# Kernel optimization log

Measured on AMD Instinct MI355X. Metric: run time of the kernel, lower is better.

Reference implementation:

```python
import jax, jax.numpy as jnp
import numpy as np

B, L, K = 4096, 4096, 10


def _sparsemax(z):
    # z: [..., n]; Martins & Astudillo sparsemax along last dim
    n = z.shape[-1]
    zs = -jnp.sort(-z, axis=-1)                      # descending
    cum = jnp.cumsum(zs, axis=-1)
    r = jnp.arange(1, n + 1, dtype=z.dtype)
    support = (1.0 + r * zs) > cum                   # [..., n]
    ksel = jnp.sum(support, axis=-1, keepdims=True)  # support size
    tau = (jnp.take_along_axis(cum, ksel - 1, axis=-1) - 1.0) / ksel.astype(z.dtype)
    return jnp.maximum(z - tau, 0.0)


def _topk_bitvectors(logits, k):
    # k highest-scoring binary vectors z in {0,1}^L under <z, logits>
    # (faithful to the CPU batched_topk: detached logits)
    lg = jax.lax.stop_gradient(logits)
    b, latent = lg.shape
    base = (lg > 0).astype(lg.dtype)                 # argmax config [B, L]
    costs = jnp.abs(lg)                              # flip costs
    neg_small, pos = jax.lax.top_k(-costs, k)        # k smallest costs + positions
    c_small = -neg_small                             # [B, k]
    m = 1 << k                                       # 2^k candidate flip subsets
    bits = ((jnp.arange(m)[:, None] >> jnp.arange(k)[None, :]) & 1).astype(lg.dtype)  # [2^k, k]
    sums = jnp.einsum('mk,bk->bm', bits, c_small)    # total flip cost per subset
    _, best = jax.lax.top_k(-sums, k)                # k cheapest subsets [B, k]
    flips = bits[best]                               # [B, k, k] which small-cost bits to flip
    base_at = jnp.take_along_axis(base, pos, axis=1) # base bit value at flip positions [B, k]
    delta = flips * (1.0 - 2.0 * base_at[:, None, :])  # +1 or -1 where flipped
    bv = jnp.broadcast_to(base[:, None, :], (b, k, latent))
    bidx = jnp.arange(b)[:, None, None]
    cidx = jnp.arange(k)[None, :, None]
    jpos = pos[:, None, :]                           # [B, 1, k]
    bv = bv.at[bidx, cidx, jpos].add(delta)          # scatter flips -> [B, k, L]
    return bv


def reference(logits, k):
    bv = _topk_bitvectors(logits, k)                         # [B, k, L]
    scores = jnp.einsum('bkj,bj->bk', bv, logits)            # [B, k]
    distr = _sparsemax(scores)                               # [B, k]
    p = distr.reshape(-1)
    safe_p = jnp.where(p > 0, p, 1.0)
    entropy = -jnp.sum(jnp.where(p > 0, p * jnp.log(safe_p), 0.0))
    batch_size = logits.shape[0]
    return bv, distr, entropy / batch_size


def setup_inputs() -> dict:
    key = jax.random.key(0)
    logits = jax.random.normal(key, (B, L), dtype=jnp.float32)
    return {"logits": logits, "k": K}
```

## Files before the change

kernel.cpp:

```cpp
#include <hip/hip_runtime.h>
#include <stdint.h>

#define NB   4096
#define LDIM 4096
#define KK   10
#define TPB  256
#define CAP  1024

typedef float fx4 __attribute__((ext_vector_type(4)));

__device__ __forceinline__ unsigned long long wave_min_u64(unsigned long long v) {
#pragma unroll
    for (int off = 1; off < 64; off <<= 1) {
        const unsigned long long o = __shfl_xor(v, off, 64);
        if (o < v) v = o;
    }
    return v;
}

__global__ __launch_bounds__(TPB) void select_rows(
    const float* __restrict__ logits,
    float* __restrict__ distr,
    float* __restrict__ entp,
    unsigned* __restrict__ meta)
{
    __shared__ float s_wsum[4];
    __shared__ int   s_pos[KK];
    __shared__ int   s_sign[KK];
    __shared__ int   s_bestm[KK];
    __shared__ int   s_cnt;
    __shared__ unsigned long long s_cand[CAP];

    const int b    = blockIdx.x;
    const int t    = threadIdx.x;
    const int lane = t & 63;
    const int wv   = t >> 6;
    const float* __restrict__ row = logits + (size_t)b * LDIM;

    float vals[16];
#pragma unroll
    for (int q = 0; q < 4; q++) {
        const float4 f = *(const float4*)(row + (q << 10) + (t << 2));
        vals[q*4+0] = f.x; vals[q*4+1] = f.y; vals[q*4+2] = f.z; vals[q*4+3] = f.w;
    }

    float s0 = 0.f;
#pragma unroll
    for (int i = 0; i < 16; i++) s0 += vals[i] > 0.f ? vals[i] : 0.f;
#pragma unroll
    for (int off = 1; off < 64; off <<= 1) s0 += __shfl_xor(s0, off, 64);
    if (lane == 0) s_wsum[wv] = s0;

    float T = 0.02f;
    int cnt = 0;
    for (int attempt = 0; attempt < 15; attempt++) {
        if (t == 0) s_cnt = 0;
        __syncthreads();
#pragma unroll
        for (int i = 0; i < 16; i++) {
            const float v    = vals[i];
            const float cost = fabsf(v);
            if (cost < T) {
                const int idx = ((i >> 2) << 10) + (t << 2) + (i & 3);
                const unsigned long long pk =
                    ((unsigned long long)__float_as_uint(cost) << 32)
                    | (unsigned)((idx << 1) | (v > 0.f ? 1 : 0));
                const int p = atomicAdd(&s_cnt, 1);
                if (p < CAP) s_cand[p] = pk;
            }
        }
        __syncthreads();
        cnt = s_cnt;
        if (cnt >= KK && cnt <= CAP) break;
        T = (cnt < KK) ? T * 4.0f : T * 0.25f;
        __syncthreads();
    }

    if (wv != 0) return;

    const float S0 = (s_wsum[0] + s_wsum[1]) + (s_wsum[2] + s_wsum[3]);
    float csm[KK];
    unsigned long long prev = 0ull;

    if (cnt >= KK && cnt <= CAP) {
        const int nc = cnt;
#pragma unroll
        for (int c = 0; c < KK; c++) {
            unsigned long long best = ~0ull;
            for (int p = lane; p < nc; p += 64) {
                const unsigned long long pk = s_cand[p];
                if ((c == 0 || pk > prev) && pk < best) best = pk;
            }
            best = wave_min_u64(best);
            prev = best;
            csm[c] = __uint_as_float((unsigned)(best >> 32));
            if (lane == 0) {
                const unsigned lo = (unsigned)best;
                s_pos[c]  = (int)(lo >> 1);
                s_sign[c] = (int)(lo & 1u);
            }
        }
    } else {
#pragma unroll
        for (int c = 0; c < KK; c++) {
            unsigned long long best = ~0ull;
            for (int p = lane; p < LDIM; p += 64) {
                const float v    = row[p];
                const float cost = fabsf(v);
                const unsigned long long pk =
                    ((unsigned long long)__float_as_uint(cost) << 32)
                    | (unsigned)((p << 1) | (v > 0.f ? 1 : 0));
                if ((c == 0 || pk > prev) && pk < best) best = pk;
            }
            best = wave_min_u64(best);
            prev = best;
            csm[c] = __uint_as_float((unsigned)(best >> 32));
            if (lane == 0) {
                const unsigned lo = (unsigned)best;
                s_pos[c]  = (int)(lo >> 1);
                s_sign[c] = (int)(lo & 1u);
            }
        }
    }

    float sums[16];
#pragma unroll
    for (int i = 0; i < 16; i++) {
        const int m = (lane << 4) | i;
        float acc = 0.f;
#pragma unroll
        for (int j = 0; j < KK; j++) acc += (m & (1 << j)) ? csm[j] : 0.f;
        sums[i] = acc;
    }

    float zc[KK];
    unsigned long long prev2 = 0ull;
#pragma unroll
    for (int c = 0; c < KK; c++) {
        unsigned long long best = ~0ull;
#pragma unroll
        for (int i = 0; i < 16; i++) {
            const unsigned long long pk =
                ((unsigned long long)__float_as_uint(sums[i]) << 32)
                | (unsigned)((lane << 4) | i);
            if ((c == 0 || pk > prev2) && pk < best) best = pk;
        }
        best = wave_min_u64(best);
        prev2 = best;
        zc[c] = S0 - __uint_as_float((unsigned)(best >> 32));
        if (lane == 0) s_bestm[c] = (int)((unsigned)best & 1023u);
    }

    if (lane == 0) {
        float acc = 0.f; int ks = 0;
#pragma unroll
        for (int r = 1; r <= KK; r++) {
            acc += zc[r-1];
            if (1.f + (float)r * zc[r-1] > acc) ks++;
        }
        float acc2 = 0.f;
#pragma unroll
        for (int r = 0; r < KK; r++) if (r < ks) acc2 += zc[r];
        const float tau = (acc2 - 1.f) / (float)ks;
        float entl = 0.f;
        float* drow = distr + b * KK;
#pragma unroll
        for (int c = 0; c < KK; c++) {
            float p = zc[c] - tau;
            p = p > 0.f ? p : 0.f;
            drow[c] = p;
            if (p > 0.f) entl -= p * logf(p);
        }
        entp[b] = entl;

        unsigned* mrow = meta + b * KK;
#pragma unroll
        for (int s = 0; s < KK; s++) {
            unsigned fm = 0u;
#pragma unroll
            for (int c = 0; c < KK; c++)
                fm |= (((unsigned)s_bestm[c] >> s) & 1u) << c;
            mrow[s] = (unsigned)s_pos[s] | (fm << 12) | ((unsigned)s_sign[s] << 22);
        }
    }
}

__global__ __launch_bounds__(TPB) void bv_writer(
    const float* __restrict__ logits,
    const unsigned* __restrict__ meta,
    float* __restrict__ bv)
{
    __shared__ unsigned s_m[KK];
    const int bid = blockIdx.x;
    const int b   = bid >> 2;
    const int seg = bid & 3;
    const int t   = threadIdx.x;
    if (t < KK) s_m[t] = meta[b * KK + t];
    __syncthreads();

    const int j0 = (seg << 10) + (t << 2);
    const float4 f = *(const float4*)(logits + (size_t)b * LDIM + j0);
    float basef[4];
    basef[0] = f.x > 0.f ? 1.f : 0.f;
    basef[1] = f.y > 0.f ? 1.f : 0.f;
    basef[2] = f.z > 0.f ? 1.f : 0.f;
    basef[3] = f.w > 0.f ? 1.f : 0.f;

    unsigned rf[4] = {0u, 0u, 0u, 0u};
    float    fv[4] = {0.f, 0.f, 0.f, 0.f};
#pragma unroll
    for (int s = 0; s < KK; s++) {
        const unsigned m   = s_m[s];
        const int      pos = (int)(m & 0xFFFu);
        const unsigned msk = (m >> 12) & 0x3FFu;
        const float    val = ((m >> 22) & 1u) ? 0.f : 1.f;
#pragma unroll
        for (int e = 0; e < 4; e++)
            if (pos == j0 + e) { rf[e] = msk; fv[e] = val; }
    }

    float* out0 = bv + (size_t)b * (KK * LDIM) + j0;
#pragma unroll
    for (int c = 0; c < KK; c++) {
        fx4 v;
        v.x = ((rf[0] >> c) & 1u) ? fv[0] : basef[0];
        v.y = ((rf[1] >> c) & 1u) ? fv[1] : basef[1];
        v.z = ((rf[2] >> c) & 1u) ? fv[2] : basef[2];
        v.w = ((rf[3] >> c) & 1u) ? fv[3] : basef[3];
        __builtin_nontemporal_store(v, (fx4*)(out0 + c * LDIM));
    }
}

__global__ __launch_bounds__(256) void ent_reduce(
    const float* __restrict__ ws, float* __restrict__ ent)
{
    __shared__ float sw[4];
    const int t = threadIdx.x, lane = t & 63, wv = t >> 6;
    float s = 0.f;
    for (int i = t; i < NB; i += 256) s += ws[i];
#pragma unroll
    for (int off = 1; off < 64; off <<= 1) s += __shfl_xor(s, off, 64);
    if (lane == 0) sw[wv] = s;
    __syncthreads();
    if (t == 0) *ent = (sw[0] + sw[1] + sw[2] + sw[3]) * (1.0f / (float)NB);
}

__global__ __launch_bounds__(TPB) void topk_sparsemax_fused(
    const float* __restrict__ logits,
    float* __restrict__ bv,
    float* __restrict__ distr,
    float* __restrict__ ent)
{
    __shared__ float s_wsum[4];
    __shared__ int   s_pos[KK];
    __shared__ int   s_sign[KK];
    __shared__ int   s_bestm[KK];
    __shared__ int   s_cnt;
    __shared__ unsigned long long s_cand[CAP];

    const int b    = blockIdx.x;
    const int t    = threadIdx.x;
    const int lane = t & 63;
    const int wv   = t >> 6;
    const float* __restrict__ row = logits + (size_t)b * LDIM;

    float vals[16];
#pragma unroll
    for (int q = 0; q < 4; q++) {
        const float4 f = *(const float4*)(row + (q << 10) + (t << 2));
        vals[q*4+0] = f.x; vals[q*4+1] = f.y; vals[q*4+2] = f.z; vals[q*4+3] = f.w;
    }

    float s0 = 0.f;
#pragma unroll
    for (int i = 0; i < 16; i++) s0 += vals[i] > 0.f ? vals[i] : 0.f;
#pragma unroll
    for (int off = 1; off < 64; off <<= 1) s0 += __shfl_xor(s0, off, 64);
    if (lane == 0) s_wsum[wv] = s0;

    float T = 0.02f;
    int cnt = 0;
    for (int attempt = 0; attempt < 15; attempt++) {
        if (t == 0) s_cnt = 0;
        __syncthreads();
#pragma unroll
        for (int i = 0; i < 16; i++) {
            const float v    = vals[i];
            const float cost = fabsf(v);
            if (cost < T) {
                const int idx = ((i >> 2) << 10) + (t << 2) + (i & 3);
                const unsigned long long pk =
                    ((unsigned long long)__float_as_uint(cost) << 32)
                    | (unsigned)((idx << 1) | (v > 0.f ? 1 : 0));
                const int p = atomicAdd(&s_cnt, 1);
                if (p < CAP) s_cand[p] = pk;
            }
        }
        __syncthreads();
        cnt = s_cnt;
        if (cnt >= KK && cnt <= CAP) break;
        T = (cnt < KK) ? T * 4.0f : T * 0.25f;
        __syncthreads();
    }

    if (wv == 0) {
        const float S0 = (s_wsum[0] + s_wsum[1]) + (s_wsum[2] + s_wsum[3]);
        float csm[KK];
        unsigned long long prev = 0ull;
        if (cnt >= KK && cnt <= CAP) {
            const int nc = cnt;
#pragma unroll
            for (int c = 0; c < KK; c++) {
                unsigned long long best = ~0ull;
                for (int p = lane; p < nc; p += 64) {
                    const unsigned long long pk = s_cand[p];
                    if ((c == 0 || pk > prev) && pk < best) best = pk;
                }
                best = wave_min_u64(best);
                prev = best;
                csm[c] = __uint_as_float((unsigned)(best >> 32));
                if (lane == 0) {
                    const unsigned lo = (unsigned)best;
                    s_pos[c]  = (int)(lo >> 1);
                    s_sign[c] = (int)(lo & 1u);
                }
            }
        } else {
#pragma unroll
            for (int c = 0; c < KK; c++) {
                unsigned long long best = ~0ull;
                for (int p = lane; p < LDIM; p += 64) {
                    const float v    = row[p];
                    const float cost = fabsf(v);
                    const unsigned long long pk =
                        ((unsigned long long)__float_as_uint(cost) << 32)
                        | (unsigned)((p << 1) | (v > 0.f ? 1 : 0));
                    if ((c == 0 || pk > prev) && pk < best) best = pk;
                }
                best = wave_min_u64(best);
                prev = best;
                csm[c] = __uint_as_float((unsigned)(best >> 32));
                if (lane == 0) {
                    const unsigned lo = (unsigned)best;
                    s_pos[c]  = (int)(lo >> 1);
                    s_sign[c] = (int)(lo & 1u);
                }
            }
        }
        float sums[16];
#pragma unroll
        for (int i = 0; i < 16; i++) {
            const int m = (lane << 4) | i;
            float acc = 0.f;
#pragma unroll
            for (int j = 0; j < KK; j++) acc += (m & (1 << j)) ? csm[j] : 0.f;
            sums[i] = acc;
        }
        float zc[KK];
        unsigned long long prev2 = 0ull;
#pragma unroll
        for (int c = 0; c < KK; c++) {
            unsigned long long best = ~0ull;
#pragma unroll
            for (int i = 0; i < 16; i++) {
                const unsigned long long pk =
                    ((unsigned long long)__float_as_uint(sums[i]) << 32)
                    | (unsigned)((lane << 4) | i);
                if ((c == 0 || pk > prev2) && pk < best) best = pk;
            }
            best = wave_min_u64(best);
            prev2 = best;
            zc[c] = S0 - __uint_as_float((unsigned)(best >> 32));
            if (lane == 0) s_bestm[c] = (int)((unsigned)best & 1023u);
        }
        if (lane == 0) {
            float acc = 0.f; int ks = 0;
#pragma unroll
            for (int r = 1; r <= KK; r++) {
                acc += zc[r-1];
                if (1.f + (float)r * zc[r-1] > acc) ks++;
            }
            float acc2 = 0.f;
#pragma unroll
            for (int r = 0; r < KK; r++) if (r < ks) acc2 += zc[r];
            const float tau = (acc2 - 1.f) / (float)ks;
            float entl = 0.f;
            float* drow = distr + b * KK;
#pragma unroll
            for (int c = 0; c < KK; c++) {
                float p = zc[c] - tau;
                p = p > 0.f ? p : 0.f;
                drow[c] = p;
                if (p > 0.f) entl -= p * logf(p);
            }
            atomicAdd(ent, entl * (1.0f / (float)NB));
        }
    }

    __syncthreads();

    unsigned fm[KK];
#pragma unroll
    for (int j = 0; j < KK; j++) {
        unsigned m = 0u;
#pragma unroll
        for (int c = 0; c < KK; c++)
            m |= (((unsigned)s_bestm[c] >> j) & 1u) << c;
        fm[j] = m;
    }
    int posr[KK], sgnr[KK];
#pragma unroll
    for (int j = 0; j < KK; j++) { posr[j] = s_pos[j]; sgnr[j] = s_sign[j]; }

    unsigned rowflip[16]; float flipval[16]; float basef[16];
#pragma unroll
    for (int i = 0; i < 16; i++) {
        const int col = ((i >> 2) << 10) + (t << 2) + (i & 3);
        unsigned rfm = 0u; float fvv = 0.f;
#pragma unroll
        for (int j = 0; j < KK; j++) {
            if (posr[j] == col) { rfm = fm[j]; fvv = sgnr[j] ? 0.f : 1.f; }
        }
        rowflip[i] = rfm; flipval[i] = fvv;
        basef[i]   = vals[i] > 0.f ? 1.f : 0.f;
    }

    float* out0 = bv + (size_t)b * (KK * LDIM);
#pragma unroll
    for (int c = 0; c < KK; c++) {
        float* orow = out0 + c * LDIM + (t << 2);
#pragma unroll
        for (int q = 0; q < 4; q++) {
            fx4 v;
            v.x = ((rowflip[q*4+0] >> c) & 1u) ? flipval[q*4+0] : basef[q*4+0];
            v.y = ((rowflip[q*4+1] >> c) & 1u) ? flipval[q*4+1] : basef[q*4+1];
            v.z = ((rowflip[q*4+2] >> c) & 1u) ? flipval[q*4+2] : basef[q*4+2];
            v.w = ((rowflip[q*4+3] >> c) & 1u) ? flipval[q*4+3] : basef[q*4+3];
            __builtin_nontemporal_store(v, (fx4*)(orow + (q << 10)));
        }
    }
}

extern "C" void kernel_launch(void* const* d_in, const int* in_sizes, int n_in,
                              void* d_out, int out_size, void* d_ws, size_t ws_size,
                              hipStream_t stream)
{
    const float* logits = (const float*)d_in[0];
    float* out   = (float*)d_out;
    float* bv    = out;
    float* distr = out + (size_t)NB * KK * LDIM;
    float* ent   = distr + (size_t)NB * KK;

    const size_t need = (size_t)NB * sizeof(float)
                      + (size_t)NB * KK * sizeof(unsigned);
    if (ws_size >= need) {
        float*    entp = (float*)d_ws;
        unsigned* meta = (unsigned*)((float*)d_ws + NB);
        select_rows<<<dim3(NB), dim3(TPB), 0, stream>>>(logits, distr, entp, meta);
        bv_writer <<<dim3(NB * 4), dim3(TPB), 0, stream>>>(logits, meta, bv);
        ent_reduce<<<dim3(1), dim3(256), 0, stream>>>(entp, ent);
    } else {
        (void)hipMemsetAsync(ent, 0, sizeof(float), stream);
        topk_sparsemax_fused<<<dim3(NB), dim3(TPB), 0, stream>>>(logits, bv, distr, ent);
    }
}
```

Measured before the change: 701.1 us.

## Pack base sign bits in select pass; bv writer reads bitmask instead of logits

```diff
diff --git a/kernel.cpp b/kernel.cpp
--- a/kernel.cpp
+++ b/kernel.cpp
@@ -22,13 +22,15 @@
     const float* __restrict__ logits,
     float* __restrict__ distr,
     float* __restrict__ entp,
-    unsigned* __restrict__ meta)
+    unsigned* __restrict__ meta,
+    unsigned* __restrict__ basebits)
 {
     __shared__ float s_wsum[4];
     __shared__ int   s_pos[KK];
     __shared__ int   s_sign[KK];
     __shared__ int   s_bestm[KK];
     __shared__ int   s_cnt;
+    __shared__ unsigned s_base[128];
     __shared__ unsigned long long s_cand[CAP];
 
     const int b    = blockIdx.x;
@@ -50,6 +52,17 @@
 #pragma unroll
     for (int off = 1; off < 64; off <<= 1) s0 += __shfl_xor(s0, off, 64);
     if (lane == 0) s_wsum[wv] = s0;
+
+    if (t < 128) s_base[t] = 0u;
+    __syncthreads();
+#pragma unroll
+    for (int q = 0; q < 4; q++) {
+        unsigned nib = 0u;
+#pragma unroll
+        for (int e = 0; e < 4; e++)
+            nib |= (vals[q*4+e] > 0.f ? 1u : 0u) << e;
+        atomicOr(&s_base[(q << 5) + (t >> 3)], nib << (4 * (t & 7)));
+    }
 
     float T = 0.02f;
     int cnt = 0;
@@ -76,6 +89,8 @@
         __syncthreads();
     }
 
+    if (t < 128) basebits[b * 128 + t] = s_base[t];
+
     if (wv != 0) return;
 
     const float S0 = (s_wsum[0] + s_wsum[1]) + (s_wsum[2] + s_wsum[3]);
@@ -186,48 +201,43 @@
 }
 
 __global__ __launch_bounds__(TPB) void bv_writer(
-    const float* __restrict__ logits,
+    const unsigned* __restrict__ basebits,
     const unsigned* __restrict__ meta,
     float* __restrict__ bv)
 {
+    __shared__ unsigned s_base[128];
     __shared__ unsigned s_m[KK];
-    const int bid = blockIdx.x;
-    const int b   = bid >> 2;
-    const int seg = bid & 3;
-    const int t   = threadIdx.x;
-    if (t < KK) s_m[t] = meta[b * KK + t];
+    const int c = blockIdx.x;
+    const int b = blockIdx.y;
+    const int t = threadIdx.x;
+
+    if (t < 128) s_base[t] = basebits[b * 128 + t];
+    else if (t < 128 + KK) s_m[t - 128] = meta[b * KK + (t - 128)];
     __syncthreads();
 
-    const int j0 = (seg << 10) + (t << 2);
-    const float4 f = *(const float4*)(logits + (size_t)b * LDIM + j0);
-    float basef[4];
-    basef[0] = f.x > 0.f ? 1.f : 0.f;
-    basef[1] = f.y > 0.f ? 1.f : 0.f;
-    basef[2] = f.z > 0.f ? 1.f : 0.f;
-    basef[3] = f.w > 0.f ? 1.f : 0.f;
-
-    unsigned rf[4] = {0u, 0u, 0u, 0u};
-    float    fv[4] = {0.f, 0.f, 0.f, 0.f};
+    unsigned bits = 0u;
+#pragma unroll
+    for (int u = 0; u < 4; u++)
+        bits |= ((s_base[(u << 5) + (t >> 3)] >> (4 * (t & 7))) & 0xFu) << (4 * u);
+
 #pragma unroll
     for (int s = 0; s < KK; s++) {
         const unsigned m   = s_m[s];
         const int      pos = (int)(m & 0xFFFu);
-        const unsigned msk = (m >> 12) & 0x3FFu;
-        const float    val = ((m >> 22) & 1u) ? 0.f : 1.f;
-#pragma unroll
-        for (int e = 0; e < 4; e++)
-            if (pos == j0 + e) { rf[e] = msk; fv[e] = val; }
-    }
-
-    float* out0 = bv + (size_t)b * (KK * LDIM) + j0;
-#pragma unroll
-    for (int c = 0; c < KK; c++) {
+        const unsigned flp = (m >> (12 + c)) & 1u;
+        if (((pos & 1023) >> 2) == t)
+            bits ^= flp << (4 * (pos >> 10) + (pos & 3));
+    }
+
+    float* out = bv + ((size_t)b * KK + c) * LDIM + (t << 2);
+#pragma unroll
+    for (int u = 0; u < 4; u++) {
         fx4 v;
-        v.x = ((rf[0] >> c) & 1u) ? fv[0] : basef[0];
-        v.y = ((rf[1] >> c) & 1u) ? fv[1] : basef[1];
-        v.z = ((rf[2] >> c) & 1u) ? fv[2] : basef[2];
-        v.w = ((rf[3] >> c) & 1u) ? fv[3] : basef[3];
-        __builtin_nontemporal_store(v, (fx4*)(out0 + c * LDIM));
+        v.x = (bits >> (4*u + 0)) & 1u ? 1.f : 0.f;
+        v.y = (bits >> (4*u + 1)) & 1u ? 1.f : 0.f;
+        v.z = (bits >> (4*u + 2)) & 1u ? 1.f : 0.f;
+        v.w = (bits >> (4*u + 3)) & 1u ? 1.f : 0.f;
+        *(fx4*)(out + (u << 10)) = v;
     }
 }
 
@@ -452,12 +462,14 @@
     float* ent   = distr + (size_t)NB * KK;
 
     const size_t need = (size_t)NB * sizeof(float)
-                      + (size_t)NB * KK * sizeof(unsigned);
+                      + (size_t)NB * KK * sizeof(unsigned)
+                      + (size_t)NB * 128 * sizeof(unsigned);
     if (ws_size >= need) {
         float*    entp = (float*)d_ws;
         unsigned* meta = (unsigned*)((float*)d_ws + NB);
-        select_rows<<<dim3(NB), dim3(TPB), 0, stream>>>(logits, distr, entp, meta);
-        bv_writer <<<dim3(NB * 4), dim3(TPB), 0, stream>>>(logits, meta, bv);
+        unsigned* bbit = meta + (size_t)NB * KK;
+        select_rows<<<dim3(NB), dim3(TPB), 0, stream>>>(logits, distr, entp, meta, bbit);
+        bv_writer <<<dim3(KK, NB), dim3(TPB), 0, stream>>>(bbit, meta, bv);
         ent_reduce<<<dim3(1), dim3(256), 0, stream>>>(entp, ent);
     } else {
         (void)hipMemsetAsync(ent, 0, sizeof(float), stream);
```

Result: slower. 716.6 us (+2.2%).
